# Performance work log

Measured on AMD Instinct MI355X. Metric: run time of the kernel, lower is better.

## Reference

```python
import jax, jax.numpy as jnp
import numpy as np

B, TX, TY, D, H, DK, DFF, L, V = 64, 200, 100, 512, 8, 64, 2048, 4, 30


def _ln(x, g, b, eps=1e-5):
    m = x.mean(-1, keepdims=True)
    v = x.var(-1, keepdims=True)  # biased, matches torch LayerNorm
    return (x - m) * jax.lax.rsqrt(v + eps) * g + b


def _mha(k_in, v_in, q_in, qkv, pw, pb, pad_mask, causal):
    # qkv: [3, H, DK, D] (torch Linear layout [out, in]); scale uses C = d_model
    scale = float(q_in.shape[-1]) ** 0.5
    Q = jnp.einsum('btd,hkd->bhtk', q_in, qkv[0])
    K = jnp.einsum('bsd,hkd->bhsk', k_in, qkv[1])
    Vv = jnp.einsum('bsd,hvd->bhsv', v_in, qkv[2])
    W = jnp.einsum('bhtk,bhsk->bhts', Q, K) / scale  # [B,H,T,S]
    if causal:
        tril = jnp.tril(jnp.ones((q_in.shape[1], k_in.shape[1]), bool))
        W = jnp.where(tril, W, -jnp.inf)
    if pad_mask is not None:
        W = jnp.where(pad_mask[:, None] == 1, -jnp.inf, W)
    A = jax.nn.softmax(W, axis=-1)
    out = jnp.einsum('bhts,bhsv->bhtv', A, Vv)
    b_, h_, t_, dv = out.shape
    out = out.transpose(0, 2, 1, 3).reshape(b_, t_, h_ * dv)  # concat heads
    return out @ pw.T + pb


def _attn_block(k, v, q, qkv, pw, pb, g, b, pad_mask, causal):
    kn, vn, qn = _ln(k, g, b), _ln(v, g, b), _ln(q, g, b)
    # NOTE: residual from the NORMED query, as in the original code
    return qn + _mha(kn, vn, qn, qkv, pw, pb, pad_mask, causal)


def _ff_block(x, w1, b1, w2, b2, g, b):
    h = jax.nn.relu(_ln(x, g, b) @ w1.T + b1)
    return x + h @ w2.T + b2


def _forward(x, y, enc_qkv, enc_proj_w, enc_proj_b, enc_ln1_g, enc_ln1_b,
             enc_ff_w1, enc_ff_b1, enc_ff_w2, enc_ff_b2, enc_ln2_g, enc_ln2_b,
             dec_sa_qkv, dec_sa_proj_w, dec_sa_proj_b, dec_ln1_g, dec_ln1_b,
             dec_ca_qkv, dec_ca_proj_w, dec_ca_proj_b, dec_ln2_g, dec_ln2_b,
             dec_ff_w1, dec_ff_b1, dec_ff_w2, dec_ff_b2, dec_ln3_g, dec_ln3_b,
             ll_w, ll_b, x_mask, y_mask):
    enc = x
    for i in range(L):
        enc = _attn_block(enc, enc, enc, enc_qkv[i], enc_proj_w[i], enc_proj_b[i],
                          enc_ln1_g[i], enc_ln1_b[i], x_mask, False)
        enc = _ff_block(enc, enc_ff_w1[i], enc_ff_b1[i], enc_ff_w2[i], enc_ff_b2[i],
                        enc_ln2_g[i], enc_ln2_b[i])
    dec = y
    for i in range(L):
        dec = _attn_block(dec, dec, dec, dec_sa_qkv[i], dec_sa_proj_w[i], dec_sa_proj_b[i],
                          dec_ln1_g[i], dec_ln1_b[i], y_mask, True)
        dec = _attn_block(enc, enc, dec, dec_ca_qkv[i], dec_ca_proj_w[i], dec_ca_proj_b[i],
                          dec_ln2_g[i], dec_ln2_b[i], None, False)
        dec = _ff_block(dec, dec_ff_w1[i], dec_ff_b1[i], dec_ff_w2[i], dec_ff_b2[i],
                        dec_ln3_g[i], dec_ln3_b[i])
    return dec @ ll_w.T + ll_b


def setup_inputs() -> dict:
    key = jax.random.key(0)
    ks = iter(jax.random.split(key, 64))

    def nrm(shape, s=0.02):
        return jax.random.normal(next(ks), shape, jnp.float32) * s

    return dict(
        x=nrm((B, TX, D), 1.0), y=nrm((B, TY, D), 1.0),
        x_mask=jnp.zeros((B, TX, TX), jnp.int32),
        y_mask=jnp.zeros((B, TY, TY), jnp.int32),
        enc_qkv=nrm((L, 3, H, DK, D)), enc_proj_w=nrm((L, D, D)), enc_proj_b=jnp.zeros((L, D)),
        enc_ln1_g=jnp.ones((L, D)), enc_ln1_b=jnp.zeros((L, D)),
        enc_ff_w1=nrm((L, DFF, D)), enc_ff_b1=jnp.zeros((L, DFF)),
        enc_ff_w2=nrm((L, D, DFF)), enc_ff_b2=jnp.zeros((L, D)),
        enc_ln2_g=jnp.ones((L, D)), enc_ln2_b=jnp.zeros((L, D)),
        dec_sa_qkv=nrm((L, 3, H, DK, D)), dec_sa_proj_w=nrm((L, D, D)), dec_sa_proj_b=jnp.zeros((L, D)),
        dec_ln1_g=jnp.ones((L, D)), dec_ln1_b=jnp.zeros((L, D)),
        dec_ca_qkv=nrm((L, 3, H, DK, D)), dec_ca_proj_w=nrm((L, D, D)), dec_ca_proj_b=jnp.zeros((L, D)),
        dec_ln2_g=jnp.ones((L, D)), dec_ln2_b=jnp.zeros((L, D)),
        dec_ff_w1=nrm((L, DFF, D)), dec_ff_b1=jnp.zeros((L, DFF)),
        dec_ff_w2=nrm((L, D, DFF)), dec_ff_b2=jnp.zeros((L, D)),
        dec_ln3_g=jnp.ones((L, D)), dec_ln3_b=jnp.zeros((L, D)),
        ll_w=nrm((V, D)), ll_b=jnp.zeros((V,)),
    )


def reference(x, y, x_mask, y_mask, enc_qkv, enc_proj_w, enc_proj_b, enc_ln1_g, enc_ln1_b,
              enc_ff_w1, enc_ff_b1, enc_ff_w2, enc_ff_b2, enc_ln2_g, enc_ln2_b,
              dec_sa_qkv, dec_sa_proj_w, dec_sa_proj_b, dec_ln1_g, dec_ln1_b,
              dec_ca_qkv, dec_ca_proj_w, dec_ca_proj_b, dec_ln2_g, dec_ln2_b,
              dec_ff_w1, dec_ff_b1, dec_ff_w2, dec_ff_b2, dec_ln3_g, dec_ln3_b,
              ll_w, ll_b):
    return _forward(x, y, enc_qkv, enc_proj_w, enc_proj_b, enc_ln1_g, enc_ln1_b,
                    enc_ff_w1, enc_ff_b1, enc_ff_w2, enc_ff_b2, enc_ln2_g, enc_ln2_b,
                    dec_sa_qkv, dec_sa_proj_w, dec_sa_proj_b, dec_ln1_g, dec_ln1_b,
                    dec_ca_qkv, dec_ca_proj_w, dec_ca_proj_b, dec_ln2_g, dec_ln2_b,
                    dec_ff_w1, dec_ff_b1, dec_ff_w2, dec_ff_b2, dec_ln3_g, dec_ln3_b,
                    ll_w, ll_b, x_mask, y_mask)
```

## Files before the change

### kernel.cpp

```cpp
#include <hip/hip_runtime.h>
#include <math.h>

#define B_SZ   64
#define TX_SZ  200
#define TY_SZ  100
#define D_MODEL 512
#define H_SZ   8
#define DK_SZ  64
#define DFF_SZ 2048
#define L_SZ   4
#define V_SZ   30

#define NEG_BIG -1.0e30f

#define PSTRF 204
#define ATT_LDSF (4 * 16 * PSTRF)

typedef unsigned short u16;
typedef __attribute__((ext_vector_type(8))) short short8;
typedef __attribute__((ext_vector_type(4))) short short4t;
typedef __attribute__((ext_vector_type(4))) float f32x4;
typedef __attribute__((ext_vector_type(4))) unsigned short u16x4;

__device__ __forceinline__ float b2f(u16 h) {
    union { unsigned int u; float f; } v; v.u = ((unsigned int)h) << 16; return v.f;
}
__device__ __forceinline__ u16 f2b(float f) {
    union { float f; unsigned int u; } v; v.f = f;
    unsigned int r = v.u + 0x7fffu + ((v.u >> 16) & 1u);
    return (u16)(r >> 16);
}

#define GLD16(gp, lp) __builtin_amdgcn_global_load_lds( \
    (const __attribute__((address_space(1))) unsigned int*)(gp), \
    (__attribute__((address_space(3))) unsigned int*)(lp), 16, 0, 0)

__global__ __launch_bounds__(256)
void castw_kernel(const float* __restrict__ in, u16* __restrict__ out, int n4) {
    int i = blockIdx.x * 256 + threadIdx.x;
    if (i < n4) {
        f32x4 v = ((const f32x4*)in)[i];
        u16x4 o;
        o.x = f2b(v.x); o.y = f2b(v.y); o.z = f2b(v.z); o.w = f2b(v.w);
        ((u16x4*)out)[i] = o;
    }
}

__global__ __launch_bounds__(256)
void maskpack_kernel(const int* __restrict__ mask, unsigned* __restrict__ bits,
                     int rows, int S, int wpr) {
    int row = blockIdx.x * 4 + (threadIdx.x >> 6);
    int lane = threadIdx.x & 63;
    if (row >= rows) return;
    const int* mr = mask + (size_t)row * S;
    unsigned* br = bits + (size_t)row * wpr;
    for (int s0 = 0; s0 < S; s0 += 64) {
        int s = s0 + lane;
        int v = (s < S) ? mr[s] : 0;
        unsigned long long bm = __ballot(v == 1);
        if (lane == 0) {
            br[s0 >> 5] = (unsigned)bm;
            if ((s0 >> 5) + 1 < wpr) br[(s0 >> 5) + 1] = (unsigned)(bm >> 32);
        }
    }
}

__global__ __launch_bounds__(256)
void vtrans_kernel(const u16* __restrict__ V, int ldv, u16* __restrict__ Vt,
                   int S, int spad) {
    __shared__ u16 t[16][72];
    const int bh = blockIdx.x;
    const int s0 = blockIdx.y * 16;
    const int h = bh & 7, b = bh >> 3;
    const int tid = threadIdx.x;
    {
        int sl = tid >> 4, c4 = (tid & 15) * 4;
        int s = s0 + sl;
        int ss = (s < S) ? s : S - 1;
        u16x4 v = *(const u16x4*)(V + (size_t)(b * S + ss) * ldv + h * 64 + c4);
        *(u16x4*)&t[sl][c4] = v;
    }
    __syncthreads();
    int d = tid >> 2, j0 = (tid & 3) * 4;
    if (s0 + j0 < spad) {
        u16x4 o;
        o.x = (s0 + j0 + 0 < S) ? t[j0 + 0][d] : (u16)0;
        o.y = (s0 + j0 + 1 < S) ? t[j0 + 1][d] : (u16)0;
        o.z = (s0 + j0 + 2 < S) ? t[j0 + 2][d] : (u16)0;
        o.w = (s0 + j0 + 3 < S) ? t[j0 + 3][d] : (u16)0;
        *(u16x4*)(Vt + ((size_t)bh * 64 + d) * spad + s0 + j0) = o;
    }
}

__global__ __launch_bounds__(256)
void ln_kernel(const float* __restrict__ in, const float* __restrict__ g,
               const float* __restrict__ b, float* outf, u16* outb, int rows) {
    int row = blockIdx.x * 4 + (threadIdx.x >> 6);
    int lane = threadIdx.x & 63;
    if (row >= rows) return;
    const f32x4* xr = (const f32x4*)(in + (size_t)row * D_MODEL);
    f32x4 v0 = xr[lane];
    f32x4 v1 = xr[lane + 64];
    float s  = v0.x + v0.y + v0.z + v0.w + v1.x + v1.y + v1.z + v1.w;
    float ss = v0.x*v0.x + v0.y*v0.y + v0.z*v0.z + v0.w*v0.w
             + v1.x*v1.x + v1.y*v1.y + v1.z*v1.z + v1.w*v1.w;
    #pragma unroll
    for (int off = 1; off < 64; off <<= 1) {
        s  += __shfl_xor(s, off, 64);
        ss += __shfl_xor(ss, off, 64);
    }
    float mean = s * (1.0f / D_MODEL);
    float var  = ss * (1.0f / D_MODEL) - mean * mean;
    float rstd = rsqrtf(var + 1e-5f);
    f32x4 g0 = ((const f32x4*)g)[lane],      g1 = ((const f32x4*)g)[lane + 64];
    f32x4 b0 = ((const f32x4*)b)[lane],      b1 = ((const f32x4*)b)[lane + 64];
    f32x4 o0, o1;
    o0.x = (v0.x - mean) * rstd * g0.x + b0.x;
    o0.y = (v0.y - mean) * rstd * g0.y + b0.y;
    o0.z = (v0.z - mean) * rstd * g0.z + b0.z;
    o0.w = (v0.w - mean) * rstd * g0.w + b0.w;
    o1.x = (v1.x - mean) * rstd * g1.x + b1.x;
    o1.y = (v1.y - mean) * rstd * g1.y + b1.y;
    o1.z = (v1.z - mean) * rstd * g1.z + b1.z;
    o1.w = (v1.w - mean) * rstd * g1.w + b1.w;
    if (outf) {
        f32x4* of = (f32x4*)(outf + (size_t)row * D_MODEL);
        of[lane] = o0; of[lane + 64] = o1;
    }
    if (outb) {
        u16x4* ob = (u16x4*)(outb + (size_t)row * D_MODEL);
        u16x4 p0, p1;
        p0.x = f2b(o0.x); p0.y = f2b(o0.y); p0.z = f2b(o0.z); p0.w = f2b(o0.w);
        p1.x = f2b(o1.x); p1.y = f2b(o1.y); p1.z = f2b(o1.z); p1.w = f2b(o1.w);
        ob[lane] = p0; ob[lane + 64] = p1;
    }
}

template<int BN>
__global__ __launch_bounds__(256)
void gemm_mfma_t(const u16* __restrict__ A, int lda,
                 const u16* __restrict__ W, int ldw,
                 float* outf, int ldcf, u16* outb, int ldcb,
                 const float* __restrict__ bias,
                 const float* __restrict__ resid, int ldr,
                 int relu, int K) {
    constexpr int NJ = BN / 32;
    __shared__ u16 Alds[128 * 32];
    __shared__ u16 Blds[BN * 32];
    const int tid  = threadIdx.x;
    const int wave = tid >> 6, lane = tid & 63;
    const int lr = lane & 15, lq = lane >> 4;
    const int wm = (wave >> 1) * 64, wn = (wave & 1) * (BN / 2);
    const int m0 = blockIdx.y * 128, n0 = blockIdx.x * BN;
    const int grow = tid >> 2;
    const int gcol = (tid & 3) * 8;
    const int woff = wave * 512;

    f32x4 zero = {0.f, 0.f, 0.f, 0.f};
    f32x4 acc[4][NJ];
    #pragma unroll
    for (int i = 0; i < 4; ++i)
        #pragma unroll
        for (int j = 0; j < NJ; ++j) acc[i][j] = zero;

    const u16* Ag = A + (size_t)m0 * lda;
    const u16* Wg = W + (size_t)n0 * ldw;

    for (int k0 = 0; k0 < K; k0 += 32) {
        GLD16(Ag + (size_t)grow * lda + k0 + gcol,        &Alds[woff]);
        GLD16(Ag + (size_t)(64 + grow) * lda + k0 + gcol, &Alds[2048 + woff]);
        GLD16(Wg + (size_t)grow * ldw + k0 + gcol,        &Blds[woff]);
        if (BN == 128)
            GLD16(Wg + (size_t)(64 + grow) * ldw + k0 + gcol, &Blds[2048 + woff]);
        __syncthreads();
        short8 af[4], bfr[NJ];
        #pragma unroll
        for (int i = 0; i < 4; ++i)
            af[i] = *(const short8*)&Alds[(wm + i * 16 + lr) * 32 + lq * 8];
        #pragma unroll
        for (int j = 0; j < NJ; ++j)
            bfr[j] = *(const short8*)&Blds[(wn + j * 16 + lr) * 32 + lq * 8];
        #pragma unroll
        for (int i = 0; i < 4; ++i)
            #pragma unroll
            for (int j = 0; j < NJ; ++j)
                acc[i][j] = __builtin_amdgcn_mfma_f32_16x16x32_bf16(af[i], bfr[j], acc[i][j], 0, 0, 0);
        __syncthreads();
    }

    #pragma unroll
    for (int i = 0; i < 4; ++i) {
        #pragma unroll
        for (int r = 0; r < 4; ++r) {
            int m = m0 + wm + i * 16 + lq * 4 + r;
            #pragma unroll
            for (int j = 0; j < NJ; ++j) {
                int n = n0 + wn + j * 16 + lr;
                float c = acc[i][j][r];
                if (bias)  c += bias[n];
                if (resid) c += resid[(size_t)m * ldr + n];
                if (relu)  c = fmaxf(c, 0.f);
                if (outf) outf[(size_t)m * ldcf + n] = c;
                if (outb) outb[(size_t)m * ldcb + n] = f2b(c);
            }
        }
    }
}

__global__ __launch_bounds__(256, 3)
void attn_kernel(u16* __restrict__ Q, int ldq, const u16* __restrict__ K, int ldk,
                 const u16* __restrict__ Vt, int spad,
                 const unsigned* __restrict__ mbits, int mwpr,
                 int T, int S, int causal, float rscale) {
    __shared__ float Pl[ATT_LDSF];
    const int bh = blockIdx.x, tile = blockIdx.y;
    const int h = bh & 7, b = bh >> 3;
    const int tid = threadIdx.x, wave = tid >> 6, lane = tid & 63;
    const int lm = lane & 15, quad = lane >> 4;
    const int t0 = tile * 64 + wave * 16;
    if (t0 >= T) return;

    const u16* Kg = K + (size_t)(b * S) * ldk + h * DK_SZ;
    const u16* Vg = Vt + (size_t)bh * 64 * spad;
    u16* Qg = Q + (size_t)(b * T) * ldq + h * DK_SZ;

    const int stiles = (S + 15) >> 4;
    int stmax = stiles;
    if (causal) { int c = (t0 >> 4) + 1; if (c < stmax) stmax = c; }
    const int Scap8 = (S + 7) & ~7;
    int Pcap = stmax * 16; if (Pcap > Scap8) Pcap = Scap8;

    float* Pw = Pl + wave * (16 * PSTRF);

    int qr = t0 + lm; if (qr >= T) qr = T - 1;
    const u16* qrow = Qg + (size_t)qr * ldq;
    short8 qa0 = *(const short8*)(qrow + quad * 8);
    short8 qa1 = *(const short8*)(qrow + 32 + quad * 8);

    const short8 zero8 = {0, 0, 0, 0, 0, 0, 0, 0};
    const f32x4 zerof = {0.f, 0.f, 0.f, 0.f};

    float mx[4] = {NEG_BIG, NEG_BIG, NEG_BIG, NEG_BIG};
    #pragma unroll
    for (int st = 0; st < 13; ++st) if (st < stmax) {
        int srow = st * 16 + lm; if (srow >= S) srow = S - 1;
        const u16* kp = Kg + (size_t)srow * ldk + quad * 8;
        short8 kb0 = *(const short8*)kp;
        short8 kb1 = *(const short8*)(kp + 32);
        f32x4 c = zerof;
        c = __builtin_amdgcn_mfma_f32_16x16x32_bf16(qa0, kb0, c, 0, 0, 0);
        c = __builtin_amdgcn_mfma_f32_16x16x32_bf16(qa1, kb1, c, 0, 0, 0);

        int s = st * 16 + lm;
        #pragma unroll
        for (int r = 0; r < 4; ++r) {
            int t = t0 + quad * 4 + r;
            int tc = (t < T) ? t : T - 1;
            bool valid = (s < S) && (!causal || s <= t);
            if (valid && mbits) {
                unsigned w = mbits[(size_t)(b * T + tc) * mwpr + (s >> 5)];
                valid = ((w >> (s & 31)) & 1u) == 0;
            }
            float f = valid ? c[r] * rscale : NEG_BIG;
            mx[r] = fmaxf(mx[r], f);
            if (s < PSTRF) Pw[(quad * 4 + r) * PSTRF + s] = f;
        }
    }
    #pragma unroll
    for (int r = 0; r < 4; ++r) {
        #pragma unroll
        for (int off = 1; off < 16; off <<= 1)
            mx[r] = fmaxf(mx[r], __shfl_xor(mx[r], off, 64));
    }

    float sum[4] = {0.f, 0.f, 0.f, 0.f};
    #pragma unroll
    for (int st = 0; st < 13; ++st) if (st < stmax) {
        int col = st * 16 + lm;
        if (col < PSTRF) {
            #pragma unroll
            for (int r = 0; r < 4; ++r) {
                int idx = (quad * 4 + r) * PSTRF + col;
                float p = __expf(Pw[idx] - mx[r]);
                sum[r] += p;
                Pw[idx] = p;
            }
        }
    }
    float rden[4];
    #pragma unroll
    for (int r = 0; r < 4; ++r) {
        #pragma unroll
        for (int off = 1; off < 16; off <<= 1)
            sum[r] += __shfl_xor(sum[r], off, 64);
        rden[r] = (sum[r] > 0.f) ? 1.0f / sum[r] : 0.f;
    }

    f32x4 ov[4] = {zerof, zerof, zerof, zerof};
    for (int k0 = 0; k0 < Pcap; k0 += 32) {
        int nq = (Pcap - k0) >> 3;
        short8 pa = zero8;
        if (quad < nq) {
            const float* prow = Pw + lm * PSTRF + k0 + quad * 8;
            f32x4 p0 = *(const f32x4*)prow;
            f32x4 p1 = *(const f32x4*)(prow + 4);
            pa[0] = (short)f2b(p0.x); pa[1] = (short)f2b(p0.y);
            pa[2] = (short)f2b(p0.z); pa[3] = (short)f2b(p0.w);
            pa[4] = (short)f2b(p1.x); pa[5] = (short)f2b(p1.y);
            pa[6] = (short)f2b(p1.z); pa[7] = (short)f2b(p1.w);
        }
        #pragma unroll
        for (int dt = 0; dt < 4; ++dt) {
            short8 vb = (quad < nq)
                ? *(const short8*)(Vg + (size_t)(dt * 16 + lm) * spad + k0 + quad * 8)
                : zero8;
            ov[dt] = __builtin_amdgcn_mfma_f32_16x16x32_bf16(pa, vb, ov[dt], 0, 0, 0);
        }
    }

    #pragma unroll
    for (int r = 0; r < 4; ++r) {
        int t = t0 + quad * 4 + r;
        if (t < T) {
            u16* orow = Qg + (size_t)t * ldq;
            #pragma unroll
            for (int dt = 0; dt < 4; ++dt)
                orow[dt * 16 + lm] = f2b(ov[dt][r] * rden[r]);
        }
    }
}

__global__ __launch_bounds__(256)
void logits_kernel(const float* __restrict__ X, const float* __restrict__ Wl,
                   const float* __restrict__ bl, float* __restrict__ out, int rows) {
    int idx = blockIdx.x * 256 + threadIdx.x;
    if (idx >= rows * V_SZ) return;
    int row = idx / V_SZ, v = idx % V_SZ;
    const f32x4* xr = (const f32x4*)(X + (size_t)row * D_MODEL);
    const f32x4* wr = (const f32x4*)(Wl + (size_t)v * D_MODEL);
    float acc = bl[v];
    #pragma unroll 4
    for (int k = 0; k < D_MODEL / 4; ++k) {
        f32x4 a = xr[k], w = wr[k];
        acc += a.x * w.x + a.y * w.y + a.z * w.z + a.w * w.w;
    }
    out[idx] = acc;
}

extern "C" void kernel_launch(void* const* d_in, const int* in_sizes, int n_in,
                              void* d_out, int out_size, void* d_ws, size_t ws_size,
                              hipStream_t stream) {
    const float* x          = (const float*)d_in[0];
    const float* y          = (const float*)d_in[1];
    const int*   x_mask     = (const int*)d_in[2];
    const int*   y_mask     = (const int*)d_in[3];
    const float* enc_qkv    = (const float*)d_in[4];
    const float* enc_proj_w = (const float*)d_in[5];
    const float* enc_proj_b = (const float*)d_in[6];
    const float* enc_ln1_g  = (const float*)d_in[7];
    const float* enc_ln1_b  = (const float*)d_in[8];
    const float* enc_ff_w1  = (const float*)d_in[9];
    const float* enc_ff_b1  = (const float*)d_in[10];
    const float* enc_ff_w2  = (const float*)d_in[11];
    const float* enc_ff_b2  = (const float*)d_in[12];
    const float* enc_ln2_g  = (const float*)d_in[13];
    const float* enc_ln2_b  = (const float*)d_in[14];
    const float* dec_sa_qkv    = (const float*)d_in[15];
    const float* dec_sa_proj_w = (const float*)d_in[16];
    const float* dec_sa_proj_b = (const float*)d_in[17];
    const float* dec_ln1_g  = (const float*)d_in[18];
    const float* dec_ln1_b  = (const float*)d_in[19];
    const float* dec_ca_qkv    = (const float*)d_in[20];
    const float* dec_ca_proj_w = (const float*)d_in[21];
    const float* dec_ca_proj_b = (const float*)d_in[22];
    const float* dec_ln2_g  = (const float*)d_in[23];
    const float* dec_ln2_b  = (const float*)d_in[24];
    const float* dec_ff_w1  = (const float*)d_in[25];
    const float* dec_ff_b1  = (const float*)d_in[26];
    const float* dec_ff_w2  = (const float*)d_in[27];
    const float* dec_ff_b2  = (const float*)d_in[28];
    const float* dec_ln3_g  = (const float*)d_in[29];
    const float* dec_ln3_b  = (const float*)d_in[30];
    const float* ll_w       = (const float*)d_in[31];
    const float* ll_b       = (const float*)d_in[32];

    const int ME = B_SZ * TX_SZ;
    const int MD = B_SZ * TY_SZ;
    const float rscale = 1.0f / sqrtf((float)D_MODEL);
    const int XWPR = (TX_SZ + 31) / 32;
    const int YWPR = (TY_SZ + 31) / 32;

    char* base = (char*)d_ws;
    size_t off = 0;
    auto alloc = [&](size_t bytes) {
        void* p = base + off;
        off = (off + bytes + 63) & ~(size_t)63;
        return p;
    };
    float* A_enc = (float*)alloc((size_t)ME * D_MODEL * 4);
    float* A_dec = (float*)alloc((size_t)MD * D_MODEL * 4);
    float* N1f   = (float*)alloc((size_t)ME * D_MODEL * 4);
    u16*   N1b   = (u16*)  alloc((size_t)ME * D_MODEL * 2);
    u16*   NQb   = (u16*)  alloc((size_t)MD * D_MODEL * 2);
    u16*   BIG   = (u16*)  alloc((size_t)ME * DFF_SZ * 2);
    u16*   Wa    = (u16*)  alloc((size_t)DFF_SZ * D_MODEL * 2);
    u16*   Wb2   = (u16*)  alloc((size_t)DFF_SZ * D_MODEL * 2);
    u16*   Vt    = (u16*)  alloc((size_t)B_SZ * H_SZ * 64 * 208 * 2);
    unsigned* XMb = (unsigned*)alloc((size_t)ME * XWPR * 4);
    unsigned* YMb = (unsigned*)alloc((size_t)MD * YWPR * 4);
    u16* QKVb = BIG;
    u16* Hb   = BIG;
    u16* KVb  = BIG;
    u16* Qca  = BIG + (size_t)ME * 1024;

    auto castw = [&](const float* in, u16* out, int n) {
        int n4 = n / 4;
        hipLaunchKernelGGL(castw_kernel, dim3((n4 + 255) / 256), dim3(256), 0, stream, in, out, n4);
    };
    auto ln = [&](const float* in, const float* g, const float* b,
                  float* outf, u16* outb, int rows) {
        hipLaunchKernelGGL(ln_kernel, dim3(rows / 4), dim3(256), 0, stream, in, g, b, outf, outb, rows);
    };
    auto gemm = [&](const u16* A, int lda, const u16* W, int ldw, int M, int N, int K,
                    float* outf, int ldcf, u16* outb, int ldcb,
                    const float* bias, const float* resid, int ldr, int relu) {
        int blocks128 = (M / 128) * (N / 128);
        if (blocks128 < 256) {
            dim3 grid(N / 64, M / 128);
            hipLaunchKernelGGL((gemm_mfma_t<64>), grid, dim3(256), 0, stream,
                               A, lda, W, ldw, outf, ldcf, outb, ldcb, bias, resid, ldr, relu, K);
        } else {
            dim3 grid(N / 128, M / 128);
            hipLaunchKernelGGL((gemm_mfma_t<128>), grid, dim3(256), 0, stream,
                               A, lda, W, ldw, outf, ldcf, outb, ldcb, bias, resid, ldr, relu, K);
        }
    };
    auto vtrans = [&](const u16* V, int ldv, int S, int spad) {
        dim3 grid(B_SZ * H_SZ, (spad + 15) / 16);
        hipLaunchKernelGGL(vtrans_kernel, grid, dim3(256), 0, stream, V, ldv, Vt, S, spad);
    };
    auto attn = [&](u16* Q, int ldq, const u16* K, int ldk, int spad,
                    const unsigned* mbits, int mwpr, int T, int S, int causal) {
        dim3 grid(B_SZ * H_SZ, (T + 63) / 64);
        hipLaunchKernelGGL(attn_kernel, grid, dim3(256), 0, stream,
                           Q, ldq, K, ldk, Vt, spad, mbits, mwpr, T, S, causal, rscale);
    };

    hipLaunchKernelGGL(maskpack_kernel, dim3((ME + 3) / 4), dim3(256), 0, stream,
                       x_mask, XMb, ME, TX_SZ, XWPR);
    hipLaunchKernelGGL(maskpack_kernel, dim3((MD + 3) / 4), dim3(256), 0, stream,
                       y_mask, YMb, MD, TY_SZ, YWPR);

    const int WQKV = 3 * D_MODEL * D_MODEL;
    const int WDD  = D_MODEL * D_MODEL;
    const int WFF  = DFF_SZ * D_MODEL;

    for (int l = 0; l < L_SZ; ++l) {
        const float* src = (l == 0) ? x : A_enc;
        castw(enc_qkv + (size_t)l * WQKV, Wa, WQKV);
        ln(src, enc_ln1_g + l * D_MODEL, enc_ln1_b + l * D_MODEL, N1f, N1b, ME);
        gemm(N1b, 512, Wa, 512, ME, 1536, 512, nullptr, 0, QKVb, 1536, nullptr, nullptr, 0, 0);
        vtrans(QKVb + 1024, 1536, TX_SZ, 200);
        attn(QKVb, 1536, QKVb + 512, 1536, 200, XMb, XWPR, TX_SZ, TX_SZ, 0);
        castw(enc_proj_w + (size_t)l * WDD, Wa, WDD);
        gemm(QKVb, 1536, Wa, 512, ME, 512, 512, A_enc, 512, nullptr, 0,
             enc_proj_b + l * D_MODEL, N1f, 512, 0);
        ln(A_enc, enc_ln2_g + l * D_MODEL, enc_ln2_b + l * D_MODEL, nullptr, N1b, ME);
        castw(enc_ff_w1 + (size_t)l * WFF, Wa, WFF);
        gemm(N1b, 512, Wa, 512, ME, 2048, 512, nullptr, 0, Hb, 2048,
             enc_ff_b1 + l * DFF_SZ, nullptr, 0, 1);
        castw(enc_ff_w2 + (size_t)l * WFF, Wb2, WFF);
        gemm(Hb, 2048, Wb2, 2048, ME, 512, 2048, A_enc, 512, nullptr, 0,
             enc_ff_b2 + l * D_MODEL, A_enc, 512, 0);
    }

    for (int l = 0; l < L_SZ; ++l) {
        const float* src = (l == 0) ? y : A_dec;
        castw(dec_sa_qkv + (size_t)l * WQKV, Wa, WQKV);
        ln(src, dec_ln1_g + l * D_MODEL, dec_ln1_b + l * D_MODEL, N1f, N1b, MD);
        gemm(N1b, 512, Wa, 512, MD, 1536, 512, nullptr, 0, QKVb, 1536, nullptr, nullptr, 0, 0);
        vtrans(QKVb + 1024, 1536, TY_SZ, 104);
        attn(QKVb, 1536, QKVb + 512, 1536, 104, YMb, YWPR, TY_SZ, TY_SZ, 1);
        castw(dec_sa_proj_w + (size_t)l * WDD, Wa, WDD);
        gemm(QKVb, 1536, Wa, 512, MD, 512, 512, A_dec, 512, nullptr, 0,
             dec_sa_proj_b + l * D_MODEL, N1f, 512, 0);
        ln(A_enc, dec_ln2_g + l * D_MODEL, dec_ln2_b + l * D_MODEL, nullptr, N1b, ME);
        ln(A_dec, dec_ln2_g + l * D_MODEL, dec_ln2_b + l * D_MODEL, N1f, NQb, MD);
        castw(dec_ca_qkv + (size_t)l * WQKV, Wa, WDD);
        gemm(NQb, 512, Wa, 512, MD, 512, 512, nullptr, 0, Qca, 512, nullptr, nullptr, 0, 0);
        castw(dec_ca_qkv + (size_t)l * WQKV + WDD, Wa, 2 * WDD);
        gemm(N1b, 512, Wa, 512, ME, 1024, 512, nullptr, 0, KVb, 1024,
             nullptr, nullptr, 0, 0);
        vtrans(KVb + 512, 1024, TX_SZ, 200);
        attn(Qca, 512, KVb, 1024, 200, nullptr, XWPR, TY_SZ, TX_SZ, 0);
        castw(dec_ca_proj_w + (size_t)l * WDD, Wa, WDD);
        gemm(Qca, 512, Wa, 512, MD, 512, 512, A_dec, 512, nullptr, 0,
             dec_ca_proj_b + l * D_MODEL, N1f, 512, 0);
        ln(A_dec, dec_ln3_g + l * D_MODEL, dec_ln3_b + l * D_MODEL, nullptr, N1b, MD);
        castw(dec_ff_w1 + (size_t)l * WFF, Wa, WFF);
        gemm(N1b, 512, Wa, 512, MD, 2048, 512, nullptr, 0, Hb, 2048,
             dec_ff_b1 + l * DFF_SZ, nullptr, 0, 1);
        castw(dec_ff_w2 + (size_t)l * WFF, Wb2, WFF);
        gemm(Hb, 2048, Wb2, 2048, MD, 512, 2048, A_dec, 512, nullptr, 0,
             dec_ff_b2 + l * D_MODEL, A_dec, 512, 0);
    }

    {
        int total = MD * V_SZ;
        hipLaunchKernelGGL(logits_kernel, dim3((total + 255) / 256), dim3(256), 0, stream,
                           A_dec, ll_w, ll_b, (float*)d_out, MD);
    }
    (void)in_sizes; (void)n_in; (void)out_size; (void)ws_size;
}
```

Measured before the change: 3.254 ms.

## Double-buffer GEMM LDS tiles and remap workgroups across XCDs

```diff
diff --git a/kernel.cpp b/kernel.cpp
--- a/kernel.cpp
+++ b/kernel.cpp
@@ -143,15 +143,17 @@
                  float* outf, int ldcf, u16* outb, int ldcb,
                  const float* __restrict__ bias,
                  const float* __restrict__ resid, int ldr,
-                 int relu, int K) {
+                 int relu, int K, int NP, int q8) {
     constexpr int NJ = BN / 32;
-    __shared__ u16 Alds[128 * 32];
-    __shared__ u16 Blds[BN * 32];
+    __shared__ u16 Alds[2][128 * 32];
+    __shared__ u16 Blds[2][BN * 32];
     const int tid  = threadIdx.x;
     const int wave = tid >> 6, lane = tid & 63;
     const int lr = lane & 15, lq = lane >> 4;
     const int wm = (wave >> 1) * 64, wn = (wave & 1) * (BN / 2);
-    const int m0 = blockIdx.y * 128, n0 = blockIdx.x * BN;
+    const int bid = blockIdx.x;
+    const int sid = q8 ? ((bid & 7) * q8 + (bid >> 3)) : bid;
+    const int m0 = (sid / NP) * 128, n0 = (sid % NP) * BN;
     const int grow = tid >> 2;
     const int gcol = (tid & 3) * 8;
     const int woff = wave * 512;
@@ -166,26 +168,34 @@
     const u16* Ag = A + (size_t)m0 * lda;
     const u16* Wg = W + (size_t)n0 * ldw;
 
-    for (int k0 = 0; k0 < K; k0 += 32) {
-        GLD16(Ag + (size_t)grow * lda + k0 + gcol,        &Alds[woff]);
-        GLD16(Ag + (size_t)(64 + grow) * lda + k0 + gcol, &Alds[2048 + woff]);
-        GLD16(Wg + (size_t)grow * ldw + k0 + gcol,        &Blds[woff]);
+    auto stage = [&](int buf, int k0) {
+        GLD16(Ag + (size_t)grow * lda + k0 + gcol,        &Alds[buf][woff]);
+        GLD16(Ag + (size_t)(64 + grow) * lda + k0 + gcol, &Alds[buf][2048 + woff]);
+        GLD16(Wg + (size_t)grow * ldw + k0 + gcol,        &Blds[buf][woff]);
         if (BN == 128)
-            GLD16(Wg + (size_t)(64 + grow) * ldw + k0 + gcol, &Blds[2048 + woff]);
-        __syncthreads();
+            GLD16(Wg + (size_t)(64 + grow) * ldw + k0 + gcol, &Blds[buf][2048 + woff]);
+    };
+
+    stage(0, 0);
+    __syncthreads();
+    const int nt = K >> 5;
+    int cur = 0;
+    for (int t = 0; t < nt; ++t) {
+        if (t + 1 < nt) stage(cur ^ 1, (t + 1) << 5);
         short8 af[4], bfr[NJ];
         #pragma unroll
         for (int i = 0; i < 4; ++i)
-            af[i] = *(const short8*)&Alds[(wm + i * 16 + lr) * 32 + lq * 8];
+            af[i] = *(const short8*)&Alds[cur][(wm + i * 16 + lr) * 32 + lq * 8];
         #pragma unroll
         for (int j = 0; j < NJ; ++j)
-            bfr[j] = *(const short8*)&Blds[(wn + j * 16 + lr) * 32 + lq * 8];
+            bfr[j] = *(const short8*)&Blds[cur][(wn + j * 16 + lr) * 32 + lq * 8];
         #pragma unroll
         for (int i = 0; i < 4; ++i)
             #pragma unroll
             for (int j = 0; j < NJ; ++j)
                 acc[i][j] = __builtin_amdgcn_mfma_f32_16x16x32_bf16(af[i], bfr[j], acc[i][j], 0, 0, 0);
         __syncthreads();
+        cur ^= 1;
     }
 
     #pragma unroll
@@ -425,14 +435,18 @@
                     float* outf, int ldcf, u16* outb, int ldcb,
                     const float* bias, const float* resid, int ldr, int relu) {
         int blocks128 = (M / 128) * (N / 128);
-        if (blocks128 < 256) {
-            dim3 grid(N / 64, M / 128);
-            hipLaunchKernelGGL((gemm_mfma_t<64>), grid, dim3(256), 0, stream,
-                               A, lda, W, ldw, outf, ldcf, outb, ldcb, bias, resid, ldr, relu, K);
+        if (blocks128 < 512) {
+            int NP = N / 64, nwg = (M / 128) * NP;
+            int q8 = (nwg % 8 == 0) ? nwg / 8 : 0;
+            hipLaunchKernelGGL((gemm_mfma_t<64>), dim3(nwg), dim3(256), 0, stream,
+                               A, lda, W, ldw, outf, ldcf, outb, ldcb, bias, resid, ldr, relu,
+                               K, NP, q8);
         } else {
-            dim3 grid(N / 128, M / 128);
-            hipLaunchKernelGGL((gemm_mfma_t<128>), grid, dim3(256), 0, stream,
-                               A, lda, W, ldw, outf, ldcf, outb, ldcb, bias, resid, ldr, relu, K);
+            int NP = N / 128, nwg = (M / 128) * NP;
+            int q8 = (nwg % 8 == 0) ? nwg / 8 : 0;
+            hipLaunchKernelGGL((gemm_mfma_t<128>), dim3(nwg), dim3(256), 0, stream,
+                               A, lda, W, ldw, outf, ldcf, outb, ldcb, bias, resid, ldr, relu,
+                               K, NP, q8);
         }
     };
     auto vtrans = [&](const u16* V, int ldv, int S, int spad) {
```

Measured after the change: 2.911 ms. -10.5%, faster.
